# Optimization experiments

Measured on AMD Instinct MI355X. Metric: run time of the kernel, lower is better.

The kernel has to match this reference:

```python
import jax, jax.numpy as jnp
import numpy as np

N, CIN, COUT, K, STY, H, W = 16, 512, 512, 3, 512, 64, 64
EPS = 1e-8
PAD = K // 2


def setup_inputs() -> dict:
    key = jax.random.key(0)
    k1, k2, k3, k4, k5, k6 = jax.random.split(key, 6)
    x = jax.random.normal(k1, (N, CIN, H, W), dtype=jnp.float32)
    style = jax.random.normal(k2, (N, STY), dtype=jnp.float32)
    noise = jax.random.normal(k3, (N, 1, H, W), dtype=jnp.float32)
    # learned parameters
    weight = jax.random.normal(k4, (1, COUT, CIN, K, K), dtype=jnp.float32)
    style_w = jax.random.normal(k5, (CIN, STY), dtype=jnp.float32) * (1.0 / np.sqrt(STY))
    style_b = jax.random.normal(k6, (CIN,), dtype=jnp.float32) * 0.01 + 1.0  # ~bias_init=1 as in StyleGAN2
    noise_weight = jnp.zeros((1,), dtype=jnp.float32)
    return {"x": x, "style": style, "noise": noise, "weight": weight,
            "style_w": style_w, "style_b": style_b, "noise_weight": noise_weight}


def _per_sample_conv(xi, wi):
    # xi: (CIN, H, W), wi: (COUT, CIN, K, K) -> (COUT, H, W)
    out = jax.lax.conv_general_dilated(
        xi[None], wi, window_strides=(1, 1),
        padding=[(PAD, PAD), (PAD, PAD)],
        dimension_numbers=("NCHW", "OIHW", "NCHW"))
    return out[0]


def reference(x, style, noise, weight, style_w, style_b, noise_weight):
    n = x.shape[0]
    # style modulation: Linear(style_channels -> in_channels), style_bias=0
    s = style @ style_w.T + style_b                     # (N, CIN)
    w = weight * s[:, None, :, None, None]              # (N, COUT, CIN, K, K)
    # demodulation
    demod = jax.lax.rsqrt(jnp.sum(w * w, axis=(2, 3, 4)) + EPS)  # (N, COUT)
    w = w * demod[:, :, None, None, None]
    # grouped conv (groups=batch) == per-sample conv, vmapped over batch
    out = jax.vmap(_per_sample_conv)(x, w)              # (N, COUT, H, W)
    # noise injection + LeakyReLU(0.2)
    out = out + noise_weight[0] * noise
    out = jnp.where(out >= 0, out, 0.2 * out)
    return out
```

## Files before the change

### kernel.cpp

```cpp
#include <hip/hip_runtime.h>
#include <hip/hip_bf16.h>
#include <stdint.h>

#define NB   16
#define CIN  512
#define COUT 512
#define STY  512
#define HH   64
#define WW   64
#define KT   9
#define KDIM (CIN*KT)
#define HP   66
#define PIX  (HH*WW)
#define EPSV 1e-8f

#define SLOT 16384
#define NKT  144

typedef __attribute__((ext_vector_type(8))) __bf16 bf16x8;
typedef __attribute__((ext_vector_type(4))) float floatx4;
typedef unsigned short ushort;

__device__ __forceinline__ ushort f32_to_bf16(float f) {
    union { float f; uint32_t u; } v; v.f = f;
    uint32_t u = v.u;
    u += 0x7fffu + ((u >> 16) & 1u);
    return (ushort)(u >> 16);
}

__device__ __forceinline__ void async16(const void* g, void* l) {
    __builtin_amdgcn_global_load_lds(
        (const __attribute__((address_space(1))) uint32_t*)g,
        (__attribute__((address_space(3))) uint32_t*)l, 16, 0, 0);
}

__global__ void __launch_bounds__(256) style_kernel(
    const float* __restrict__ style, const float* __restrict__ style_w,
    const float* __restrict__ style_b, float* __restrict__ s) {
    const int n = blockIdx.x;
    const int ci = blockIdx.y * 64 + (threadIdx.x >> 2);
    const int q = threadIdx.x & 3;
    const float4* wv = (const float4*)(style_w + (size_t)ci * STY);
    const float4* sv = (const float4*)(style + (size_t)n * STY);
    float acc = 0.f;
    #pragma unroll 8
    for (int j = q; j < STY / 4; j += 4) {
        float4 a = wv[j], b = sv[j];
        acc += a.x * b.x + a.y * b.y + a.z * b.z + a.w * b.w;
    }
    acc += __shfl_down(acc, 2, 4);
    acc += __shfl_down(acc, 1, 4);
    if (q == 0) s[(size_t)n * CIN + ci] = acc + style_b[ci];
}

__global__ void __launch_bounds__(256) modw_kernel(
    const float* __restrict__ weight, const float* __restrict__ s,
    ushort* __restrict__ Wt) {
    __shared__ float wL[KDIM];
    __shared__ float sL[CIN];
    __shared__ float red[4];
    const int co = blockIdx.x, n = blockIdx.y, t = threadIdx.x;
    const float2* wv = (const float2*)(weight + (size_t)co * KDIM);
    float2* wLv = (float2*)wL;
    #pragma unroll
    for (int i = 0; i < 9; ++i) wLv[t + 256 * i] = wv[t + 256 * i];
    ((float2*)sL)[t] = ((const float2*)(s + (size_t)n * CIN))[t];
    __syncthreads();
    float m[18];
    float sum = 0.f;
    #pragma unroll
    for (int c = 0; c < 2; ++c) {
        int ci = 2 * t + c;
        float sm = sL[ci];
        #pragma unroll
        for (int kk = 0; kk < 9; ++kk) {
            float v = wL[ci * 9 + kk] * sm;
            m[c * 9 + kk] = v;
            sum += v * v;
        }
    }
    for (int off = 32; off > 0; off >>= 1) sum += __shfl_down(sum, off, 64);
    if ((t & 63) == 0) red[t >> 6] = sum;
    __syncthreads();
    const float demod = rsqrtf(red[0] + red[1] + red[2] + red[3] + EPSV);
    uint32_t* orow = (uint32_t*)(Wt + (size_t)(n * COUT + co) * KDIM);
    #pragma unroll
    for (int kk = 0; kk < 9; ++kk) {
        uint32_t lo = (uint32_t)f32_to_bf16(m[kk] * demod);
        uint32_t hi = (uint32_t)f32_to_bf16(m[9 + kk] * demod);
        orow[kk * 256 + t] = lo | (hi << 16);
    }
}

__global__ void __launch_bounds__(256) zborder_kernel(unsigned long long* __restrict__ xt8) {
    int idx = blockIdx.x * 256 + threadIdx.x;
    int k = idx & 127;
    int rem = idx >> 7;
    int slot = rem % 260;
    int n = rem / 260;
    int hp, wp;
    if (slot < 66)       { hp = 0;  wp = slot; }
    else if (slot < 132) { hp = 65; wp = slot - 66; }
    else { int r = slot - 132; hp = 1 + (r >> 1); wp = (r & 1) ? 65 : 0; }
    xt8[(size_t)((n * HP + hp) * HP + wp) * 128 + k] = 0ull;
}

__global__ void __launch_bounds__(256) xpose_kernel(
    const float* __restrict__ x, ushort* __restrict__ xt) {
    const int h = blockIdx.x;
    const int n = blockIdx.y;
    const int t = threadIdx.x;
    __shared__ float tile[64][68];
    for (int ci0 = 0; ci0 < CIN; ci0 += 64) {
        #pragma unroll
        for (int r = 0; r < 4; ++r) {
            int cil = r * 16 + (t >> 4);
            int w4 = (t & 15) * 4;
            float4 v = *(const float4*)&x[(((size_t)n * CIN + ci0 + cil) * HH + h) * WW + w4];
            *(float4*)&tile[cil][w4] = v;
        }
        __syncthreads();
        #pragma unroll
        for (int r = 0; r < 8; ++r) {
            int w = (t >> 5) + r * 8;
            int cil = 2 * (t & 31);
            uint32_t lo = (uint32_t)f32_to_bf16(tile[cil][w]);
            uint32_t hi = (uint32_t)f32_to_bf16(tile[cil + 1][w]);
            *(uint32_t*)&xt[(((size_t)n * HP + h + 1) * HP + (w + 1)) * CIN + ci0 + cil] =
                lo | (hi << 16);
        }
        __syncthreads();
    }
}

template<int VMC, bool STAGE>
__device__ __forceinline__ void ktile(
    int kt, short* lds_, const ushort* __restrict__ Wt, const ushort* __restrict__ xt,
    size_t gA0, size_t gA1, size_t gB0, size_t gB1,
    int dA0, int dA1, int dB0, int dB1,
    int aBase, int bBase, floatx4 (&acc)[8][4]) {
    short* sbase = lds_ + (kt & 3) * SLOT;
    __builtin_amdgcn_sched_barrier(0);
    if constexpr (VMC == 8)      asm volatile("s_waitcnt vmcnt(8)" ::: "memory");
    else if constexpr (VMC == 4) asm volatile("s_waitcnt vmcnt(4)" ::: "memory");
    else                         asm volatile("s_waitcnt vmcnt(0)" ::: "memory");
    __builtin_amdgcn_s_barrier();
    __builtin_amdgcn_sched_barrier(0);

    bf16x8 a0[4], a1[4], bv[4];
    #pragma unroll
    for (int i = 0; i < 4; ++i) a0[i] = *(const bf16x8*)(sbase + aBase + i * 512);
    #pragma unroll
    for (int i = 0; i < 4; ++i) bv[i] = *(const bf16x8*)(sbase + bBase + i * 512);
    #pragma unroll
    for (int i = 0; i < 4; ++i) a1[i] = *(const bf16x8*)(sbase + aBase + 2048 + i * 512);
    if constexpr (STAGE) {
        short* dbase = lds_ + ((kt + 3) & 3) * SLOT;
        size_t offA = (size_t)(kt + 3) * 32;
        async16(Wt + gA0 + offA, dbase + dA0);
        async16(Wt + gA1 + offA, dbase + dA1);
        int ktp = kt + 3;
        int tap = ktp >> 4;
        int kh = tap / 3, kw = tap - kh * 3;
        size_t offB = (size_t)(kh * HP + kw) * CIN + (size_t)((ktp & 15) << 5);
        async16(xt + gB0 + offB, dbase + dB0);
        async16(xt + gB1 + offB, dbase + dB1);
    }
    __builtin_amdgcn_s_setprio(1);
    #pragma unroll
    for (int mi = 0; mi < 4; ++mi)
        #pragma unroll
        for (int ni = 0; ni < 4; ++ni)
            acc[mi][ni] = __builtin_amdgcn_mfma_f32_16x16x32_bf16(
                a0[mi], bv[ni], acc[mi][ni], 0, 0, 0);
    #pragma unroll
    for (int mi = 0; mi < 4; ++mi)
        #pragma unroll
        for (int ni = 0; ni < 4; ++ni)
            acc[4 + mi][ni] = __builtin_amdgcn_mfma_f32_16x16x32_bf16(
                a1[mi], bv[ni], acc[4 + mi][ni], 0, 0, 0);
    __builtin_amdgcn_s_setprio(0);
}

__global__ void __launch_bounds__(512, 2) conv_kernel(
    const ushort* __restrict__ Wt, const ushort* __restrict__ xt,
    const float* __restrict__ noise, const float* __restrict__ nw_p,
    float* __restrict__ out) {
    __shared__ short lds[4 * SLOT];
    const int t = threadIdx.x;
    const int bid = blockIdx.x;
    const int xcd = bid & 7;
    const int slot = bid >> 3;
    const int p = slot & 15;
    const int pg = xcd * 4 + (slot >> 4);
    const int n = pg >> 1;
    const int co0 = (pg & 1) * 256;
    const int pos0 = p * 256;
    const int h0 = p * 4;

    const int l = t & 63;
    const int wv = t >> 6;
    const int wr = wv >> 2;
    const int wc = wv & 3;
    const int lrow = l & 15;
    const int lkg = l >> 4;
    const int kcol = (lkg ^ ((l >> 1) & 3)) * 8;
    const int aBase = (wr * 128 + lrow) * 32 + kcol;
    const int bBase = 8192 + (wc * 64 + lrow) * 32 + kcol;

    size_t gAq[2], gBq[2];
    int dAq[2], dBq[2];
    #pragma unroll
    for (int q = 0; q < 2; ++q) {
        int e = q * 4096 + t * 8;
        int row = e >> 5;
        int gr = (e >> 3) & 3;
        int grs = gr ^ ((row >> 1) & 3);
        gAq[q] = (size_t)(n * COUT + co0 + row) * KDIM + grs * 8;
        int prow = row >> 6, pcol = row & 63;
        gBq[q] = ((size_t)(n * HP + h0 + prow) * HP + pcol) * CIN + grs * 8;
        dAq[q] = q * 4096 + t * 8;
        dBq[q] = 8192 + q * 4096 + t * 8;
    }

    floatx4 acc[8][4];
    #pragma unroll
    for (int i = 0; i < 8; ++i)
        #pragma unroll
        for (int j = 0; j < 4; ++j) acc[i][j] = (floatx4){0.f, 0.f, 0.f, 0.f};

    #pragma unroll
    for (int ktp = 0; ktp < 3; ++ktp) {
        short* dbase = lds + ktp * SLOT;
        size_t off = (size_t)ktp * 32;
        async16(Wt + gAq[0] + off, dbase + dAq[0]);
        async16(Wt + gAq[1] + off, dbase + dAq[1]);
        async16(xt + gBq[0] + off, dbase + dBq[0]);
        async16(xt + gBq[1] + off, dbase + dBq[1]);
    }

    #pragma unroll 1
    for (int kt = 0; kt < 141; ++kt)
        ktile<8, true>(kt, lds, Wt, xt, gAq[0], gAq[1], gBq[0], gBq[1],
                       dAq[0], dAq[1], dBq[0], dBq[1], aBase, bBase, acc);
    ktile<8, false>(141, lds, Wt, xt, gAq[0], gAq[1], gBq[0], gBq[1],
                    dAq[0], dAq[1], dBq[0], dBq[1], aBase, bBase, acc);
    ktile<4, false>(142, lds, Wt, xt, gAq[0], gAq[1], gBq[0], gBq[1],
                    dAq[0], dAq[1], dBq[0], dBq[1], aBase, bBase, acc);
    ktile<0, false>(143, lds, Wt, xt, gAq[0], gAq[1], gBq[0], gBq[1],
                    dAq[0], dAq[1], dBq[0], dBq[1], aBase, bBase, acc);

    const float nwv = nw_p[0];
    float nz[4];
    #pragma unroll
    for (int ni = 0; ni < 4; ++ni)
        nz[ni] = nwv * noise[(size_t)n * PIX + pos0 + wc * 64 + ni * 16 + lrow];
    #pragma unroll
    for (int mi = 0; mi < 8; ++mi) {
        #pragma unroll
        for (int r = 0; r < 4; ++r) {
            int cout = co0 + wr * 128 + mi * 16 + lkg * 4 + r;
            float* orow = out + ((size_t)n * COUT + cout) * PIX + pos0 + wc * 64;
            #pragma unroll
            for (int ni = 0; ni < 4; ++ni) {
                float v = acc[mi][ni][r] + nz[ni];
                v = v >= 0.f ? v : 0.2f * v;
                orow[ni * 16 + lrow] = v;
            }
        }
    }
}

extern "C" void kernel_launch(void* const* d_in, const int* in_sizes, int n_in,
                              void* d_out, int out_size, void* d_ws, size_t ws_size,
                              hipStream_t stream) {
    const float* x       = (const float*)d_in[0];
    const float* style   = (const float*)d_in[1];
    const float* noise   = (const float*)d_in[2];
    const float* weight  = (const float*)d_in[3];
    const float* style_w = (const float*)d_in[4];
    const float* style_b = (const float*)d_in[5];
    const float* noise_w = (const float*)d_in[6];
    float* out = (float*)d_out;

    char* ws = (char*)d_ws;
    ushort* Wt = (ushort*)ws;
    ushort* xt = (ushort*)(ws + 75497472);
    float*  s  = (float*)(ws + 75497472 + 71368704);

    hipLaunchKernelGGL(style_kernel,   dim3(16, 8),    dim3(256), 0, stream,
                       style, style_w, style_b, s);
    hipLaunchKernelGGL(modw_kernel,    dim3(512, 16),  dim3(256), 0, stream,
                       weight, s, Wt);
    hipLaunchKernelGGL(zborder_kernel, dim3(2080),     dim3(256), 0, stream,
                       (unsigned long long*)xt);
    hipLaunchKernelGGL(xpose_kernel,   dim3(64, 16),   dim3(256), 0, stream,
                       x, xt);
    hipLaunchKernelGGL(conv_kernel,    dim3(512),      dim3(512), 0, stream,
                       Wt, xt, noise, noise_w, out);
}
```

Before: 530.6 us.

## Prefetch next k-tile B fragments from LDS mid-iteration with register ping-pong

The loop now loads the next k-tile's B fragments from LDS into registers between the two MFMA halves of the current tile. It alternates two register sets, so that LDS read latency overlaps with matrix math instead of stalling at the start of each tile. To make the next slot safe to read early, the global-load wait is tightened from vmcnt(8) to vmcnt(4). That shortens the effective async prefetch depth and adds register pressure. The loop is manually unrolled by two, with a prologue and an adjusted tail.

Measured after the change: 547.9 us. +3.2%, slower.

```diff
diff --git a/kernel.cpp b/kernel.cpp
--- a/kernel.cpp
+++ b/kernel.cpp
@@ -133,25 +133,23 @@
     }
 }
 
-template<int VMC, bool STAGE>
-__device__ __forceinline__ void ktile(
+template<int VMC, bool STAGE, bool PREFETCH>
+__device__ __forceinline__ void ktile2(
     int kt, short* lds_, const ushort* __restrict__ Wt, const ushort* __restrict__ xt,
     size_t gA0, size_t gA1, size_t gB0, size_t gB1,
     int dA0, int dA1, int dB0, int dB1,
-    int aBase, int bBase, floatx4 (&acc)[8][4]) {
+    int aBase, int bBase,
+    bf16x8 (&bv)[4], bf16x8 (&ax)[4], bf16x8 (&a1)[4],
+    floatx4 (&acc)[8][4]) {
     short* sbase = lds_ + (kt & 3) * SLOT;
     __builtin_amdgcn_sched_barrier(0);
-    if constexpr (VMC == 8)      asm volatile("s_waitcnt vmcnt(8)" ::: "memory");
-    else if constexpr (VMC == 4) asm volatile("s_waitcnt vmcnt(4)" ::: "memory");
-    else                         asm volatile("s_waitcnt vmcnt(0)" ::: "memory");
+    if constexpr (VMC == 4) asm volatile("s_waitcnt vmcnt(4)" ::: "memory");
+    else                    asm volatile("s_waitcnt vmcnt(0)" ::: "memory");
     __builtin_amdgcn_s_barrier();
     __builtin_amdgcn_sched_barrier(0);
 
-    bf16x8 a0[4], a1[4], bv[4];
-    #pragma unroll
-    for (int i = 0; i < 4; ++i) a0[i] = *(const bf16x8*)(sbase + aBase + i * 512);
-    #pragma unroll
-    for (int i = 0; i < 4; ++i) bv[i] = *(const bf16x8*)(sbase + bBase + i * 512);
+    #pragma unroll
+    for (int i = 0; i < 4; ++i) ax[i] = *(const bf16x8*)(sbase + aBase + i * 512);
     #pragma unroll
     for (int i = 0; i < 4; ++i) a1[i] = *(const bf16x8*)(sbase + aBase + 2048 + i * 512);
     if constexpr (STAGE) {
@@ -172,7 +170,14 @@
         #pragma unroll
         for (int ni = 0; ni < 4; ++ni)
             acc[mi][ni] = __builtin_amdgcn_mfma_f32_16x16x32_bf16(
-                a0[mi], bv[ni], acc[mi][ni], 0, 0, 0);
+                ax[mi], bv[ni], acc[mi][ni], 0, 0, 0);
+    __builtin_amdgcn_s_setprio(0);
+    if constexpr (PREFETCH) {
+        short* nb = lds_ + ((kt + 1) & 3) * SLOT;
+        #pragma unroll
+        for (int i = 0; i < 4; ++i) ax[i] = *(const bf16x8*)(nb + bBase + i * 512);
+    }
+    __builtin_amdgcn_s_setprio(1);
     #pragma unroll
     for (int mi = 0; mi < 4; ++mi)
         #pragma unroll
@@ -239,16 +244,28 @@
         async16(xt + gBq[1] + off, dbase + dBq[1]);
     }
 
+    bf16x8 P[4], Q[4], R[4];
+
+    asm volatile("s_waitcnt vmcnt(8)" ::: "memory");
+    __builtin_amdgcn_s_barrier();
+    #pragma unroll
+    for (int i = 0; i < 4; ++i) P[i] = *(const bf16x8*)(lds + bBase + i * 512);
+
     #pragma unroll 1
-    for (int kt = 0; kt < 141; ++kt)
-        ktile<8, true>(kt, lds, Wt, xt, gAq[0], gAq[1], gBq[0], gBq[1],
-                       dAq[0], dAq[1], dBq[0], dBq[1], aBase, bBase, acc);
-    ktile<8, false>(141, lds, Wt, xt, gAq[0], gAq[1], gBq[0], gBq[1],
-                    dAq[0], dAq[1], dBq[0], dBq[1], aBase, bBase, acc);
-    ktile<4, false>(142, lds, Wt, xt, gAq[0], gAq[1], gBq[0], gBq[1],
-                    dAq[0], dAq[1], dBq[0], dBq[1], aBase, bBase, acc);
-    ktile<0, false>(143, lds, Wt, xt, gAq[0], gAq[1], gBq[0], gBq[1],
-                    dAq[0], dAq[1], dBq[0], dBq[1], aBase, bBase, acc);
+    for (int j = 0; j < 70; ++j) {
+        ktile2<4, true, true>(2 * j, lds, Wt, xt, gAq[0], gAq[1], gBq[0], gBq[1],
+                              dAq[0], dAq[1], dBq[0], dBq[1], aBase, bBase, P, Q, R, acc);
+        ktile2<4, true, true>(2 * j + 1, lds, Wt, xt, gAq[0], gAq[1], gBq[0], gBq[1],
+                              dAq[0], dAq[1], dBq[0], dBq[1], aBase, bBase, Q, P, R, acc);
+    }
+    ktile2<4, true,  true >(140, lds, Wt, xt, gAq[0], gAq[1], gBq[0], gBq[1],
+                            dAq[0], dAq[1], dBq[0], dBq[1], aBase, bBase, P, Q, R, acc);
+    ktile2<4, false, true >(141, lds, Wt, xt, gAq[0], gAq[1], gBq[0], gBq[1],
+                            dAq[0], dAq[1], dBq[0], dBq[1], aBase, bBase, Q, P, R, acc);
+    ktile2<0, false, true >(142, lds, Wt, xt, gAq[0], gAq[1], gBq[0], gBq[1],
+                            dAq[0], dAq[1], dBq[0], dBq[1], aBase, bBase, P, Q, R, acc);
+    ktile2<0, false, false>(143, lds, Wt, xt, gAq[0], gAq[1], gBq[0], gBq[1],
+                            dAq[0], dAq[1], dBq[0], dBq[1], aBase, bBase, Q, P, R, acc);
 
     const float nwv = nw_p[0];
     float nz[4];
```
